# Kernel tuning notes

Measured on AMD Instinct MI355X. Metric: run time of the kernel, lower is better.

## Reference

```python
import jax, jax.numpy as jnp
import numpy as np

LAMBDA_COORD = 5.0
LAMBDA_NOOBJ = 0.5
EPS = 1e-16


def setup_inputs() -> dict:
    key = jax.random.key(0)
    k1, k2, k3 = jax.random.split(key, 3)
    B, HW, C = 64, 6400, 85  # 80x80 grid, 5 + 80 classes
    T = 50                   # objects per image
    predictions = jax.random.normal(k1, (B, HW, C), dtype=jnp.float32)
    targets_box = jax.random.uniform(k2, (B, T, 4), dtype=jnp.float32)  # cx, cy, w, h in [0,1)
    targets_cls = jax.random.randint(k3, (B, T), 0, 80)
    return {
        "predictions": predictions,
        "targets_box": targets_box,
        "targets_cls": targets_cls,
        "grid_h": 80,
        "grid_w": 80,
    }


def reference(predictions, targets_box, targets_cls, grid_h, grid_w):
    B, HW, C = predictions.shape
    T = targets_box.shape[1]
    H, W = grid_h, grid_w

    cx, cy, w, h = (targets_box[..., i] for i in range(4))  # each [B, T]
    gxf = jnp.floor(cx * W)
    gyf = jnp.floor(cy * H)
    gi = (gyf * W + gxf).astype(jnp.int32)  # [B, T] grid cell index

    # gather predictions at assigned cells -> [B, T, C]
    g = jnp.take_along_axis(predictions, gi[:, :, None], axis=1)

    # coordinate losses (per-object mean over the 2 components, as F.mse_loss does)
    txy = jnp.stack([cx * W - gxf, cy * H - gyf], axis=-1)           # [B, T, 2]
    xy_loss = jnp.mean((jax.nn.sigmoid(g[..., :2]) - txy) ** 2, -1)  # [B, T]
    twh = jnp.log(jnp.stack([w * W, h * H], axis=-1) + EPS)
    wh_loss = jnp.mean((g[..., 2:4] - twh) ** 2, -1)

    # objectness BCE with target 1: -log(sigmoid(p)) = softplus(-p)
    conf_loss = jax.nn.softplus(-g[..., 4])

    # class cross-entropy
    logp = jax.nn.log_softmax(g[..., 5:], axis=-1)
    cls_loss = -jnp.take_along_axis(logp, targets_cls[..., None], axis=-1)[..., 0]

    per_obj = LAMBDA_COORD * (xy_loss + wh_loss) + conf_loss + cls_loss
    obj_sum = jnp.sum(per_obj)

    # no-object loss: mean BCE(sigmoid(conf), 0) = softplus(p) over cells without objects
    obj_mask = jnp.zeros((B, HW), dtype=bool).at[jnp.arange(B)[:, None], gi].set(True)
    noobj = ~obj_mask
    sp = jax.nn.softplus(predictions[..., 4])  # [B, HW]
    noobj_per_img = jnp.sum(sp * noobj, -1) / jnp.maximum(jnp.sum(noobj, -1), 1)
    noobj_sum = LAMBDA_NOOBJ * jnp.sum(noobj_per_img)

    num_objects = B * T  # all targets are in-grid by construction
    return (obj_sum + noobj_sum) / num_objects
```

## Files before the change

kernel.cpp:

```cpp
#include <hip/hip_runtime.h>
#include <math.h>

constexpr int B_  = 64;
constexpr int HW_ = 6400;
constexpr int C_  = 85;
constexpr int T_  = 50;
constexpr int H_  = 80;
constexpr int W_  = 80;
constexpr float LC    = 5.0f;
constexpr float LN    = 0.5f;
constexpr float INV_N = 1.0f / (B_ * T_);

constexpr int OBJ_BLOCKS  = (B_ * T_) / 4;
constexpr int SUBN        = 16;
constexpr int CONF_BLOCKS = B_ * SUBN;
constexpr int CHUNK       = HW_ / SUBN;

constexpr int OFF_PEROBJ = 0;
constexpr int OFF_MSP    = OFF_PEROBJ + B_ * T_;
constexpr int OFF_CANON  = OFF_MSP + B_ * T_;
constexpr int OFF_PART   = OFF_CANON + B_ * T_;

__device__ __forceinline__ float softplus_f(float x) {
    return fmaxf(x, 0.0f) + log1pf(expf(-fabsf(x)));
}

__global__ __launch_bounds__(256) void main_kernel(
    const float* __restrict__ pred, const float* __restrict__ tbox,
    const int* __restrict__ tcls,
    float* __restrict__ per_obj, float* __restrict__ masked_sp,
    float* __restrict__ canon, float* __restrict__ img_part)
{
    if (blockIdx.x < OBJ_BLOCKS) {
        int gid  = blockIdx.x * 256 + threadIdx.x;
        int obj  = gid >> 6;
        int lane = threadIdx.x & 63;
        int b   = obj / T_;
        int myt = obj % T_;

        const float4 tb = ((const float4*)tbox)[obj];
        float gxf = floorf(tb.x * (float)W_);
        float gyf = floorf(tb.y * (float)H_);
        int gi = (int)(gyf * (float)W_ + gxf);

        bool dup = false;
        if (lane < T_) {
            const float4 to = ((const float4*)tbox)[b * T_ + lane];
            int gio = (int)(floorf(to.y * (float)H_) * (float)W_ +
                            floorf(to.x * (float)W_));
            dup = (lane < myt) && (gio == gi);
        }
        bool canonical = (__ballot(dup) == 0ULL);

        const float* g = pred + ((size_t)b * HW_ + gi) * C_;
        int cls = tcls[obj];

        int   c2 = lane + 64;
        float v1 = g[lane];
        float v2 = (c2 < C_) ? g[c2] : 0.0f;

        float m = -1e30f;
        if (lane >= 5) m = v1;
        if (c2 < C_)   m = fmaxf(m, v2);
        #pragma unroll
        for (int off = 32; off; off >>= 1) m = fmaxf(m, __shfl_xor(m, off, 64));
        float s = 0.0f;
        if (lane >= 5) s += expf(v1 - m);
        if (c2 < C_)   s += expf(v2 - m);
        #pragma unroll
        for (int off = 32; off; off >>= 1) s += __shfl_xor(s, off, 64);
        float lse = m + logf(s);

        float contrib = 0.0f;
        if (lane == 0) {
            float d = 1.0f / (1.0f + expf(-v1)) - (tb.x * (float)W_ - gxf);
            contrib = LC * 0.5f * d * d;
        } else if (lane == 1) {
            float d = 1.0f / (1.0f + expf(-v1)) - (tb.y * (float)H_ - gyf);
            contrib = LC * 0.5f * d * d;
        } else if (lane == 2) {
            float d = v1 - logf(tb.z * (float)W_ + 1e-16f);
            contrib = LC * 0.5f * d * d;
        } else if (lane == 3) {
            float d = v1 - logf(tb.w * (float)H_ + 1e-16f);
            contrib = LC * 0.5f * d * d;
        } else if (lane == 4) {
            contrib = softplus_f(-v1);
            masked_sp[obj] = canonical ? softplus_f(v1) : 0.0f;
        }
        if (lane == 5 + cls) contrib += lse - v1;
        if (c2   == 5 + cls) contrib += lse - v2;

        #pragma unroll
        for (int off = 32; off; off >>= 1) contrib += __shfl_xor(contrib, off, 64);
        if (lane == 0) {
            per_obj[obj] = contrib;
            canon[obj]   = canonical ? 1.0f : 0.0f;
        }
    } else {
        int c    = blockIdx.x - OBJ_BLOCKS;
        int b    = c >> 4;
        int sub  = c & 15;
        int base = sub * CHUNK;
        const float* p = pred + (size_t)b * HW_ * C_;

        float sum = 0.0f;
        for (int i = base + (int)threadIdx.x; i < base + CHUNK; i += 256)
            sum += softplus_f(p[(size_t)i * C_ + 4]);
        #pragma unroll
        for (int off = 32; off; off >>= 1) sum += __shfl_xor(sum, off, 64);

        __shared__ float ss[4];
        int wid = threadIdx.x >> 6;
        if ((threadIdx.x & 63) == 0) ss[wid] = sum;
        __syncthreads();
        if (threadIdx.x == 0)
            img_part[c] = ss[0] + ss[1] + ss[2] + ss[3];
    }
}

__global__ __launch_bounds__(256) void combine_kernel(
    const float* __restrict__ per_obj, const float* __restrict__ masked_sp,
    const float* __restrict__ canon, const float* __restrict__ img_part,
    float* __restrict__ out)
{
    int t = threadIdx.x;
    int b = t >> 2;
    int q = t & 3;

    float po = 0.0f, msp = 0.0f, cn = 0.0f, tp = 0.0f;
    for (int i = q; i < T_; i += 4) {
        po  += per_obj[b * T_ + i];
        msp += masked_sp[b * T_ + i];
        cn  += canon[b * T_ + i];
    }
    for (int j = q; j < SUBN; j += 4)
        tp += img_part[b * SUBN + j];

    #pragma unroll
    for (int off = 1; off <= 2; off <<= 1) {
        po  += __shfl_xor(po,  off, 64);
        msp += __shfl_xor(msp, off, 64);
        cn  += __shfl_xor(cn,  off, 64);
        tp  += __shfl_xor(tp,  off, 64);
    }

    __shared__ float simg[B_];
    if (q == 0) {
        float n_noobj = fmaxf((float)HW_ - cn, 1.0f);
        simg[b] = po + LN * (tp - msp) / n_noobj;
    }
    __syncthreads();

    if (t < 64) {
        float v = simg[t];
        #pragma unroll
        for (int off = 32; off; off >>= 1) v += __shfl_xor(v, off, 64);
        if (t == 0) out[0] = v * INV_N;
    }
}

extern "C" void kernel_launch(void* const* d_in, const int* in_sizes, int n_in,
                              void* d_out, int out_size, void* d_ws, size_t ws_size,
                              hipStream_t stream) {
    const float* pred = (const float*)d_in[0];
    const float* tbox = (const float*)d_in[1];
    const int*   tcls = (const int*)d_in[2];
    float* out = (float*)d_out;

    float* ws        = (float*)d_ws;
    float* per_obj   = ws + OFF_PEROBJ;
    float* masked_sp = ws + OFF_MSP;
    float* canon     = ws + OFF_CANON;
    float* img_part  = ws + OFF_PART;

    main_kernel<<<OBJ_BLOCKS + CONF_BLOCKS, 256, 0, stream>>>(
        pred, tbox, tcls, per_obj, masked_sp, canon, img_part);
    combine_kernel<<<1, 256, 0, stream>>>(per_obj, masked_sp, canon, img_part, out);
}
```

Baseline: 19.96 us.

## Fold per-image noobj normalization into main kernel; flatten final reduction

Each block now computes the per-image duplicate mask itself with a wave-wide shuffle loop, so it can normalize its own noobj partial and object terms by the no-object count. The final kernel becomes a flat float4 sum over a single partial array. The confidence scan uses 1600 blocks each covering one cell per thread instead of 1024 blocks that loop. This shortens the tail reduction and raises parallelism, but every block repeats a 49-step shuffle loop over the image's targets.

```diff
diff --git a/kernel.cpp b/kernel.cpp
--- a/kernel.cpp
+++ b/kernel.cpp
@@ -11,30 +11,64 @@
 constexpr float LN    = 0.5f;
 constexpr float INV_N = 1.0f / (B_ * T_);
 
-constexpr int OBJ_BLOCKS  = (B_ * T_) / 4;
-constexpr int SUBN        = 16;
-constexpr int CONF_BLOCKS = B_ * SUBN;
-constexpr int CHUNK       = HW_ / SUBN;
-
-constexpr int OFF_PEROBJ = 0;
-constexpr int OFF_MSP    = OFF_PEROBJ + B_ * T_;
-constexpr int OFF_CANON  = OFF_MSP + B_ * T_;
-constexpr int OFF_PART   = OFF_CANON + B_ * T_;
+constexpr int CHUNKS_PER_IMG = 25;
+constexpr int SCAN_BLOCKS    = B_ * CHUNKS_PER_IMG;
+constexpr int OBJ_BLOCKS     = (B_ * T_) / 4;
+constexpr int GRID_A         = SCAN_BLOCKS + OBJ_BLOCKS;
+constexpr int NPART          = SCAN_BLOCKS + B_ * T_;
 
 __device__ __forceinline__ float softplus_f(float x) {
     return fmaxf(x, 0.0f) + log1pf(expf(-fabsf(x)));
 }
 
+__device__ __forceinline__ unsigned long long dup_mask_for_image(
+    const float* __restrict__ tbox, int b, int lane)
+{
+    int gio;
+    if (lane < T_) {
+        const float4 to = ((const float4*)tbox)[b * T_ + lane];
+        gio = (int)(floorf(to.y * (float)H_) * (float)W_ +
+                    floorf(to.x * (float)W_));
+    } else {
+        gio = 0x40000000 + lane;
+    }
+    bool dup = false;
+    #pragma unroll
+    for (int k = 0; k < T_ - 1; ++k) {
+        int gk = __shfl(gio, k, 64);
+        dup = dup || ((lane > k) && (gio == gk));
+    }
+    return __ballot(dup);
+}
+
 __global__ __launch_bounds__(256) void main_kernel(
     const float* __restrict__ pred, const float* __restrict__ tbox,
-    const int* __restrict__ tcls,
-    float* __restrict__ per_obj, float* __restrict__ masked_sp,
-    float* __restrict__ canon, float* __restrict__ img_part)
+    const int* __restrict__ tcls, float* __restrict__ partial)
 {
-    if (blockIdx.x < OBJ_BLOCKS) {
-        int gid  = blockIdx.x * 256 + threadIdx.x;
-        int obj  = gid >> 6;
-        int lane = threadIdx.x & 63;
+    int lane = threadIdx.x & 63;
+    int wid  = threadIdx.x >> 6;
+    __shared__ float ss[4];
+
+    if (blockIdx.x < SCAN_BLOCKS) {
+        int c   = blockIdx.x;
+        int b   = c / CHUNKS_PER_IMG;
+        int sub = c % CHUNKS_PER_IMG;
+
+        unsigned long long dm = dup_mask_for_image(tbox, b, lane);
+        int n_unique = T_ - __popcll(dm);
+        float nn = fmaxf((float)(HW_ - n_unique), 1.0f);
+
+        int cell = sub * 256 + (int)threadIdx.x;
+        float conf = pred[((size_t)b * HW_ + cell) * C_ + 4];
+        float s = softplus_f(conf);
+        #pragma unroll
+        for (int off = 32; off; off >>= 1) s += __shfl_xor(s, off, 64);
+        if (lane == 0) ss[wid] = s;
+        __syncthreads();
+        if (threadIdx.x == 0)
+            partial[c] = LN * (ss[0] + ss[1] + ss[2] + ss[3]) / nn;
+    } else {
+        int obj = (blockIdx.x - SCAN_BLOCKS) * 4 + wid;
         int b   = obj / T_;
         int myt = obj % T_;
 
@@ -43,14 +77,10 @@
         float gyf = floorf(tb.y * (float)H_);
         int gi = (int)(gyf * (float)W_ + gxf);
 
-        bool dup = false;
-        if (lane < T_) {
-            const float4 to = ((const float4*)tbox)[b * T_ + lane];
-            int gio = (int)(floorf(to.y * (float)H_) * (float)W_ +
-                            floorf(to.x * (float)W_));
-            dup = (lane < myt) && (gio == gi);
-        }
-        bool canonical = (__ballot(dup) == 0ULL);
+        unsigned long long dm = dup_mask_for_image(tbox, b, lane);
+        bool canonical = !((dm >> myt) & 1ULL);
+        int n_unique = T_ - __popcll(dm);
+        float nn = fmaxf((float)(HW_ - n_unique), 1.0f);
 
         const float* g = pred + ((size_t)b * HW_ + gi) * C_;
         int cls = tcls[obj];
@@ -86,78 +116,35 @@
             contrib = LC * 0.5f * d * d;
         } else if (lane == 4) {
             contrib = softplus_f(-v1);
-            masked_sp[obj] = canonical ? softplus_f(v1) : 0.0f;
+            if (canonical) contrib -= LN * softplus_f(v1) / nn;
         }
         if (lane == 5 + cls) contrib += lse - v1;
         if (c2   == 5 + cls) contrib += lse - v2;
 
         #pragma unroll
         for (int off = 32; off; off >>= 1) contrib += __shfl_xor(contrib, off, 64);
-        if (lane == 0) {
-            per_obj[obj] = contrib;
-            canon[obj]   = canonical ? 1.0f : 0.0f;
-        }
-    } else {
-        int c    = blockIdx.x - OBJ_BLOCKS;
-        int b    = c >> 4;
-        int sub  = c & 15;
-        int base = sub * CHUNK;
-        const float* p = pred + (size_t)b * HW_ * C_;
-
-        float sum = 0.0f;
-        for (int i = base + (int)threadIdx.x; i < base + CHUNK; i += 256)
-            sum += softplus_f(p[(size_t)i * C_ + 4]);
-        #pragma unroll
-        for (int off = 32; off; off >>= 1) sum += __shfl_xor(sum, off, 64);
-
-        __shared__ float ss[4];
-        int wid = threadIdx.x >> 6;
-        if ((threadIdx.x & 63) == 0) ss[wid] = sum;
-        __syncthreads();
-        if (threadIdx.x == 0)
-            img_part[c] = ss[0] + ss[1] + ss[2] + ss[3];
+        if (lane == 0) partial[SCAN_BLOCKS + obj] = contrib;
     }
 }
 
-__global__ __launch_bounds__(256) void combine_kernel(
-    const float* __restrict__ per_obj, const float* __restrict__ masked_sp,
-    const float* __restrict__ canon, const float* __restrict__ img_part,
-    float* __restrict__ out)
+__global__ __launch_bounds__(256) void reduce_kernel(
+    const float* __restrict__ partial, float* __restrict__ out)
 {
-    int t = threadIdx.x;
-    int b = t >> 2;
-    int q = t & 3;
+    const float4* p4 = (const float4*)partial;
+    float s = 0.0f;
+    for (int i = threadIdx.x; i < NPART / 4; i += 256) {
+        float4 v = p4[i];
+        s += (v.x + v.y) + (v.z + v.w);
+    }
+    #pragma unroll
+    for (int off = 32; off; off >>= 1) s += __shfl_xor(s, off, 64);
 
-    float po = 0.0f, msp = 0.0f, cn = 0.0f, tp = 0.0f;
-    for (int i = q; i < T_; i += 4) {
-        po  += per_obj[b * T_ + i];
-        msp += masked_sp[b * T_ + i];
-        cn  += canon[b * T_ + i];
-    }
-    for (int j = q; j < SUBN; j += 4)
-        tp += img_part[b * SUBN + j];
-
-    #pragma unroll
-    for (int off = 1; off <= 2; off <<= 1) {
-        po  += __shfl_xor(po,  off, 64);
-        msp += __shfl_xor(msp, off, 64);
-        cn  += __shfl_xor(cn,  off, 64);
-        tp  += __shfl_xor(tp,  off, 64);
-    }
-
-    __shared__ float simg[B_];
-    if (q == 0) {
-        float n_noobj = fmaxf((float)HW_ - cn, 1.0f);
-        simg[b] = po + LN * (tp - msp) / n_noobj;
-    }
+    __shared__ float ss[4];
+    int wid = threadIdx.x >> 6;
+    if ((threadIdx.x & 63) == 0) ss[wid] = s;
     __syncthreads();
-
-    if (t < 64) {
-        float v = simg[t];
-        #pragma unroll
-        for (int off = 32; off; off >>= 1) v += __shfl_xor(v, off, 64);
-        if (t == 0) out[0] = v * INV_N;
-    }
+    if (threadIdx.x == 0)
+        out[0] = (ss[0] + ss[1] + ss[2] + ss[3]) * INV_N;
 }
 
 extern "C" void kernel_launch(void* const* d_in, const int* in_sizes, int n_in,
@@ -167,14 +154,8 @@
     const float* tbox = (const float*)d_in[1];
     const int*   tcls = (const int*)d_in[2];
     float* out = (float*)d_out;
+    float* partial = (float*)d_ws;
 
-    float* ws        = (float*)d_ws;
-    float* per_obj   = ws + OFF_PEROBJ;
-    float* masked_sp = ws + OFF_MSP;
-    float* canon     = ws + OFF_CANON;
-    float* img_part  = ws + OFF_PART;
-
-    main_kernel<<<OBJ_BLOCKS + CONF_BLOCKS, 256, 0, stream>>>(
-        pred, tbox, tcls, per_obj, masked_sp, canon, img_part);
-    combine_kernel<<<1, 256, 0, stream>>>(per_obj, masked_sp, canon, img_part, out);
+    main_kernel<<<GRID_A, 256, 0, stream>>>(pred, tbox, tcls, partial);
+    reduce_kernel<<<1, 256, 0, stream>>>(partial, out);
 }
```

New measurement: 20.82 us. 4.3% more time.
